# Kernel tuning notes

Hardware: AMD Instinct MI355X
Metric: run time of the kernel (lower is better)

The kernel has to match this reference:

```python
import jax, jax.numpy as jnp
import numpy as np

B, M, D, L = 16384, 16, 128, 26  # words, word length, feature dim, num labels


def setup_inputs() -> dict:
    key = jax.random.key(0)
    k1, k2, k3, k4 = jax.random.split(key, 4)
    X = jax.random.normal(k1, (B, M, D), dtype=jnp.float32)
    Y = jax.random.randint(k2, (B, M), 0, L, dtype=jnp.int64)
    W = jax.random.normal(k3, (L, D), dtype=jnp.float32) * 0.1
    T = jax.random.normal(k4, (L, L), dtype=jnp.float32) * 0.1
    return {"X": X, "Y": Y, "W": W, "T": T}


def reference(X, Y, W, T):
    # Negative conditional log-likelihood of a linear-chain CRF (get_crf_obj).
    # emissions: e[b, s, k] = <W[k], X[b, s]>
    emit = jnp.einsum('bsd,kd->bsk', X, W)  # [B, M, L]
    bsz = X.shape[0]

    # forward recurrence: alpha[i, j] = logsumexp_k(emit[i-1, k] + T[k, j] + alpha[i-1, k])
    def step(alpha, e_prev):
        # alpha, e_prev: [B, L]; T: [L(k), L(j)]
        new = jax.nn.logsumexp(alpha[:, :, None] + e_prev[:, :, None] + T[None, :, :], axis=1)
        return new, None

    alpha0 = jnp.zeros((bsz, emit.shape[-1]), dtype=emit.dtype)
    # scan over positions 0..M-2 (emissions at the previous step)
    alpha_last, _ = jax.lax.scan(step, alpha0, jnp.moveaxis(emit[:, :-1, :], 1, 0))

    # log partition: logsumexp_k(emit[M-1, k] + alpha[M-1, k])
    log_z = jax.nn.logsumexp(emit[:, -1, :] + alpha_last, axis=-1)  # [B]

    # node potential: sum_s emit[s, Y[s]]
    node = jnp.take_along_axis(emit, Y[:, :, None], axis=2)[:, :, 0].sum(axis=1)  # [B]
    # edge potential: sum_s T[Y[s], Y[s+1]]
    edge = T[Y[:, :-1], Y[:, 1:]].sum(axis=1)  # [B]

    log_likelihood = jnp.sum(node + edge - log_z)
    return -log_likelihood
```

## Files before the change

kernel.cpp:

```cpp
#include <hip/hip_runtime.h>
#include <math.h>


#define B_TOT 16384
#define M_LEN 16
#define D_DIM 128
#define L_LAB 26
#define WPB 4
#define NBLOCKS (B_TOT / (WPB * 2))
#define LOG2E 1.4426950408889634f
#define LN2   0.6931471805599453f
#define DELTA 5.7f
#define ESTR 36

typedef short v8s __attribute__((ext_vector_type(8)));
typedef float v4f __attribute__((ext_vector_type(4)));

static __device__ __forceinline__ unsigned bf16u(float f) {
    unsigned u = __float_as_uint(f);
    u += 0x7fff + ((u >> 16) & 1);
    return u >> 16;
}
static __device__ __forceinline__ unsigned pkbf(float lo, float hi) {
    return bf16u(lo) | (bf16u(hi) << 16);
}
static __device__ __forceinline__ float fexp2(float x) {
#if __has_builtin(__builtin_amdgcn_exp2f)
    return __builtin_amdgcn_exp2f(x);
#else
    return exp2f(x);
#endif
}
static __device__ __forceinline__ float flog2(float x) {
#if __has_builtin(__builtin_amdgcn_logf)
    return __builtin_amdgcn_logf(x);
#else
    return log2f(x);
#endif
}

__global__ void prep_kernel(const float* __restrict__ W, const float* __restrict__ T,
                            uint4* __restrict__ wsW, float* __restrict__ wsP) {
    const int l = threadIdx.x;
    const int c16 = l & 15, quad = l >> 4;
    #pragma unroll
    for (int f = 0; f < 8; ++f) {
        const int tile = f >> 2, kk = f & 3;
        const int label = tile * 16 + c16;
        const int base = kk * 32 + quad * 8;
        unsigned d[4];
        #pragma unroll
        for (int p = 0; p < 4; ++p) {
            float a = 0.f, bb = 0.f;
            if (label < L_LAB) {
                a  = W[label * D_DIM + base + 2 * p]     * LOG2E;
                bb = W[label * D_DIM + base + 2 * p + 1] * LOG2E;
            }
            d[p] = pkbf(a, bb);
        }
        wsW[l * 8 + f] = make_uint4(d[0], d[1], d[2], d[3]);
    }
    for (int i = l; i < 1024; i += 64) {
        const int j = i >> 5, k = i & 31;
        wsP[i] = (j < L_LAB && k < L_LAB)
               ? exp2f(T[k * L_LAB + j] * LOG2E - DELTA) : 0.f;
    }
}

__global__ __launch_bounds__(256, 4) void crf_kernel(
    const float* __restrict__ X, const int* __restrict__ Y,
    const float* __restrict__ T, const uint4* __restrict__ wsW,
    const float* __restrict__ wsP, float* __restrict__ out)
{
    const int lane = threadIdx.x & 63;
    const int wave = threadIdx.x >> 6;
    const int g = lane >> 5;
    const int j = lane & 31;
    const int c16 = lane & 15;
    const int quad = lane >> 4;

    __shared__ float Ts[L_LAB * L_LAB];
    __shared__ float Ee[WPB][2][M_LEN * ESTR];
    __shared__ float vrow[WPB][2][32];
    __shared__ float red[WPB];

    for (int i = threadIdx.x; i < L_LAB * L_LAB; i += 256) Ts[i] = T[i];

    uint4 wf[8];
    #pragma unroll
    for (int f = 0; f < 8; ++f) wf[f] = wsW[lane * 8 + f];

    __syncthreads();

    const int wgid = blockIdx.x * WPB + wave;

    #pragma unroll
    for (int g2 = 0; g2 < 2; ++g2) {
        const float* xb = X + (size_t)(wgid * 2 + g2) * (M_LEN * D_DIM);
        v4f acc0 = {0.f, 0.f, 0.f, 0.f};
        v4f acc1 = {0.f, 0.f, 0.f, 0.f};
        #pragma unroll
        for (int kk = 0; kk < 4; ++kk) {
            const float4* xp = (const float4*)(xb + c16 * D_DIM + kk * 32 + quad * 8);
            float4 xa = xp[0];
            float4 xc = xp[1];
            uint4 au = make_uint4(pkbf(xa.x, xa.y), pkbf(xa.z, xa.w),
                                  pkbf(xc.x, xc.y), pkbf(xc.z, xc.w));
            v8s af = *(v8s*)&au;
            v8s b0 = *(v8s*)&wf[kk];
            v8s b1 = *(v8s*)&wf[4 + kk];
            acc0 = __builtin_amdgcn_mfma_f32_16x16x32_bf16(af, b0, acc0, 0, 0, 0);
            acc1 = __builtin_amdgcn_mfma_f32_16x16x32_bf16(af, b1, acc1, 0, 0, 0);
        }
        #pragma unroll
        for (int r = 0; r < 4; ++r) {
            const int s = quad * 4 + r;
            Ee[wave][g2][s * ESTR + c16]      = fexp2(acc0[r]);
            Ee[wave][g2][s * ESTR + 16 + c16] = fexp2(acc1[r]);
        }
    }

    float4 Pc4[7];
    {
        const float4* pp = (const float4*)(wsP + j * 32);
        #pragma unroll
        for (int t = 0; t < 7; ++t) Pc4[t] = pp[t];
    }
    float Ejs[15];
    #pragma unroll
    for (int s = 1; s < M_LEN; ++s) Ejs[s - 1] = Ee[wave][g][s * ESTR + j];

    float ne = 0.f;
    if (j < M_LEN) {
        const int bb = wgid * 2 + g;
        const int ys = Y[bb * M_LEN + j];
        ne = flog2(Ee[wave][g][j * ESTR + ys]) * LN2;
        if (j < M_LEN - 1) {
            const int yn = Y[bb * M_LEN + j + 1];
            ne += Ts[ys * L_LAB + yn];
        }
    }
    ne += __shfl_xor(ne, 8);
    ne += __shfl_xor(ne, 4);
    ne += __shfl_xor(ne, 2);
    ne += __shfl_xor(ne, 1);

    float4 v4[7];
    {
        const float4* e0 = (const float4*)&Ee[wave][g][0];
        #pragma unroll
        for (int t = 0; t < 7; ++t) v4[t] = e0[t];
    }
    #pragma unroll
    for (int s = 1; s < M_LEN; ++s) {
        float4 u4 = make_float4(0.f, 0.f, 0.f, 0.f);
        #pragma unroll
        for (int t = 0; t < 7; ++t) {
            u4.x = fmaf(v4[t].x, Pc4[t].x, u4.x);
            u4.y = fmaf(v4[t].y, Pc4[t].y, u4.y);
            u4.z = fmaf(v4[t].z, Pc4[t].z, u4.z);
            u4.w = fmaf(v4[t].w, Pc4[t].w, u4.w);
        }
        const float u = (u4.x + u4.z) + (u4.y + u4.w);
        vrow[wave][g][j] = u * Ejs[s - 1];
        const float4* vr = (const float4*)&vrow[wave][g][0];
        #pragma unroll
        for (int t = 0; t < 7; ++t) v4[t] = vr[t];
    }

    float4 sv = make_float4(0.f, 0.f, 0.f, 0.f);
    #pragma unroll
    for (int t = 0; t < 7; ++t) {
        sv.x += v4[t].x; sv.y += v4[t].y; sv.z += v4[t].z; sv.w += v4[t].w;
    }
    const float logz = (flog2((sv.x + sv.z) + (sv.y + sv.w)) + 15.f * DELTA) * LN2;

    float local = logz - ne;
    const float other = __shfl(local, 32);
    if (lane == 0) red[wave] = local + other;
    __syncthreads();
    if (threadIdx.x == 0) atomicAdd(out, (red[0] + red[1]) + (red[2] + red[3]));
}

extern "C" void kernel_launch(void* const* d_in, const int* in_sizes, int n_in,
                              void* d_out, int out_size, void* d_ws, size_t ws_size,
                              hipStream_t stream) {
    const float* X = (const float*)d_in[0];
    const int*   Y = (const int*)d_in[1];
    const float* W = (const float*)d_in[2];
    const float* T = (const float*)d_in[3];
    float* out = (float*)d_out;
    uint4* wsW = (uint4*)d_ws;
    float* wsP = (float*)((char*)d_ws + 8192);

    hipMemsetAsync(out, 0, sizeof(float), stream);
    prep_kernel<<<1, 64, 0, stream>>>(W, T, wsW, wsP);
    crf_kernel<<<NBLOCKS, 256, 0, stream>>>(X, Y, T, wsW, wsP, out);
}
```

Measured before the change: 213.3 us.

## Replace LDS-based alpha recurrence with DPP row-rotation across interleaved lanes

The forward recurrence now keeps one alpha value per lane, with the two words interleaved on odd and even lanes. Each step rotates values through the row using DPP row_ror, and the transition matrix is pre-permuted into a per-lane rotated layout so the lanes can do the dot product. This removes the per-step LDS write and read of the alpha row along with its implicit wave synchronization. In exchange it adds 31 DPP moves per step and a 32-register P array, and DPP row rotation only spans 16 lanes, which makes the correctness of the rotation scheme questionable.

```diff
diff --git a/kernel.cpp b/kernel.cpp
--- a/kernel.cpp
+++ b/kernel.cpp
@@ -39,8 +39,17 @@
 #endif
 }
 
+static __device__ __forceinline__ int ror2i(int x) {
+    x = __builtin_amdgcn_update_dpp(0, x, 0x13C, 0xF, 0xF, true);
+    x = __builtin_amdgcn_update_dpp(0, x, 0x13C, 0xF, 0xF, true);
+    return x;
+}
+static __device__ __forceinline__ float ror2f(float x) {
+    return __int_as_float(ror2i(__float_as_int(x)));
+}
+
 __global__ void prep_kernel(const float* __restrict__ W, const float* __restrict__ T,
-                            uint4* __restrict__ wsW, float* __restrict__ wsP) {
+                            uint4* __restrict__ wsW, float* __restrict__ wsPr) {
     const int l = threadIdx.x;
     const int c16 = l & 15, quad = l >> 4;
     #pragma unroll
@@ -60,28 +69,29 @@
         }
         wsW[l * 8 + f] = make_uint4(d[0], d[1], d[2], d[3]);
     }
-    for (int i = l; i < 1024; i += 64) {
-        const int j = i >> 5, k = i & 31;
-        wsP[i] = (j < L_LAB && k < L_LAB)
-               ? exp2f(T[k * L_LAB + j] * LOG2E - DELTA) : 0.f;
+    const int k = l >> 1;
+    int rk = k;
+    for (int t = 0; t < 32; ++t) {
+        wsPr[l * 32 + t] = (rk < L_LAB && k < L_LAB)
+            ? exp2f(T[rk * L_LAB + k] * LOG2E - DELTA) : 0.f;
+        rk = ror2i(rk);
     }
 }
 
 __global__ __launch_bounds__(256, 4) void crf_kernel(
     const float* __restrict__ X, const int* __restrict__ Y,
     const float* __restrict__ T, const uint4* __restrict__ wsW,
-    const float* __restrict__ wsP, float* __restrict__ out)
+    const float* __restrict__ wsPr, float* __restrict__ out)
 {
     const int lane = threadIdx.x & 63;
     const int wave = threadIdx.x >> 6;
-    const int g = lane >> 5;
-    const int j = lane & 31;
+    const int k = lane >> 1;
+    const int g = lane & 1;
     const int c16 = lane & 15;
     const int quad = lane >> 4;
 
     __shared__ float Ts[L_LAB * L_LAB];
     __shared__ float Ee[WPB][2][M_LEN * ESTR];
-    __shared__ float vrow[WPB][2][32];
     __shared__ float red[WPB];
 
     for (int i = threadIdx.x; i < L_LAB * L_LAB; i += 256) Ts[i] = T[i];
@@ -120,64 +130,64 @@
         }
     }
 
-    float4 Pc4[7];
+    float Pr[32];
     {
-        const float4* pp = (const float4*)(wsP + j * 32);
-        #pragma unroll
-        for (int t = 0; t < 7; ++t) Pc4[t] = pp[t];
-    }
+        const float4* pp = (const float4*)(wsPr + lane * 32);
+        #pragma unroll
+        for (int t8 = 0; t8 < 8; ++t8) {
+            float4 q = pp[t8];
+            Pr[4 * t8 + 0] = q.x; Pr[4 * t8 + 1] = q.y;
+            Pr[4 * t8 + 2] = q.z; Pr[4 * t8 + 3] = q.w;
+        }
+    }
+
     float Ejs[15];
     #pragma unroll
-    for (int s = 1; s < M_LEN; ++s) Ejs[s - 1] = Ee[wave][g][s * ESTR + j];
+    for (int s = 1; s < M_LEN; ++s) Ejs[s - 1] = Ee[wave][g][s * ESTR + k];
+    float v = Ee[wave][g][k];
 
     float ne = 0.f;
-    if (j < M_LEN) {
-        const int bb = wgid * 2 + g;
-        const int ys = Y[bb * M_LEN + j];
-        ne = flog2(Ee[wave][g][j * ESTR + ys]) * LN2;
-        if (j < M_LEN - 1) {
-            const int yn = Y[bb * M_LEN + j + 1];
+    if (lane < 32) {
+        const int s = lane >> 1;
+        const int b = wgid * 2 + g;
+        const int ys = Y[b * M_LEN + s];
+        ne = flog2(Ee[wave][g][s * ESTR + ys]) * LN2;
+        if (s < M_LEN - 1) {
+            const int yn = Y[b * M_LEN + s + 1];
             ne += Ts[ys * L_LAB + yn];
         }
     }
+    ne += __shfl_xor(ne, 32);
+    ne += __shfl_xor(ne, 16);
     ne += __shfl_xor(ne, 8);
     ne += __shfl_xor(ne, 4);
     ne += __shfl_xor(ne, 2);
-    ne += __shfl_xor(ne, 1);
-
-    float4 v4[7];
-    {
-        const float4* e0 = (const float4*)&Ee[wave][g][0];
-        #pragma unroll
-        for (int t = 0; t < 7; ++t) v4[t] = e0[t];
-    }
+
     #pragma unroll
     for (int s = 1; s < M_LEN; ++s) {
-        float4 u4 = make_float4(0.f, 0.f, 0.f, 0.f);
-        #pragma unroll
-        for (int t = 0; t < 7; ++t) {
-            u4.x = fmaf(v4[t].x, Pc4[t].x, u4.x);
-            u4.y = fmaf(v4[t].y, Pc4[t].y, u4.y);
-            u4.z = fmaf(v4[t].z, Pc4[t].z, u4.z);
-            u4.w = fmaf(v4[t].w, Pc4[t].w, u4.w);
-        }
-        const float u = (u4.x + u4.z) + (u4.y + u4.w);
-        vrow[wave][g][j] = u * Ejs[s - 1];
-        const float4* vr = (const float4*)&vrow[wave][g][0];
-        #pragma unroll
-        for (int t = 0; t < 7; ++t) v4[t] = vr[t];
-    }
-
-    float4 sv = make_float4(0.f, 0.f, 0.f, 0.f);
-    #pragma unroll
-    for (int t = 0; t < 7; ++t) {
-        sv.x += v4[t].x; sv.y += v4[t].y; sv.z += v4[t].z; sv.w += v4[t].w;
-    }
-    const float logz = (flog2((sv.x + sv.z) + (sv.y + sv.w)) + 15.f * DELTA) * LN2;
+        float vr = v;
+        float u0 = 0.f, u1 = 0.f;
+        #pragma unroll
+        for (int t = 0; t < 32; t += 2) {
+            u0 = fmaf(vr, Pr[t], u0);
+            vr = ror2f(vr);
+            u1 = fmaf(vr, Pr[t + 1], u1);
+            if (t < 30) vr = ror2f(vr);
+        }
+        v = (u0 + u1) * Ejs[s - 1];
+    }
+
+    float tot = v;
+    tot += __shfl_xor(tot, 32);
+    tot += __shfl_xor(tot, 16);
+    tot += __shfl_xor(tot, 8);
+    tot += __shfl_xor(tot, 4);
+    tot += __shfl_xor(tot, 2);
+    const float logz = (flog2(tot) + 15.f * DELTA) * LN2;
 
     float local = logz - ne;
-    const float other = __shfl(local, 32);
-    if (lane == 0) red[wave] = local + other;
+    const float pair = local + __shfl_xor(local, 1);
+    if (lane == 0) red[wave] = pair;
     __syncthreads();
     if (threadIdx.x == 0) atomicAdd(out, (red[0] + red[1]) + (red[2] + red[3]));
 }
@@ -190,10 +200,10 @@
     const float* W = (const float*)d_in[2];
     const float* T = (const float*)d_in[3];
     float* out = (float*)d_out;
-    uint4* wsW = (uint4*)d_ws;
-    float* wsP = (float*)((char*)d_ws + 8192);
+    uint4* wsW  = (uint4*)d_ws;
+    float* wsPr = (float*)((char*)d_ws + 8192);
 
     hipMemsetAsync(out, 0, sizeof(float), stream);
-    prep_kernel<<<1, 64, 0, stream>>>(W, T, wsW, wsP);
-    crf_kernel<<<NBLOCKS, 256, 0, stream>>>(X, Y, T, wsW, wsP, out);
-}
+    prep_kernel<<<1, 64, 0, stream>>>(W, T, wsW, wsPr);
+    crf_kernel<<<NBLOCKS, 256, 0, stream>>>(X, Y, T, wsW, wsPr, out);
+}
```

New measurement: 225.3 us. 1.06x slower.
